# Optimization experiments

Hardware: AMD Instinct MI355X
Metric: run time of the kernel (lower is better)

## Reference

```python
import jax, jax.numpy as jnp
import numpy as np


def setup_inputs() -> dict:
    key = jax.random.key(0)
    ks = jax.random.split(key, 6)
    E, N, S = 6, 4096, 64
    std_b = (2.0 / (S + S)) ** 0.5
    std_a = (2.0 / (S + S)) ** 0.5
    return {
        "x": jax.random.normal(ks[0], (1, N, S), dtype=jnp.float32),
        "edge_matrix": jax.random.uniform(ks[1], (E, N, N), dtype=jnp.float32),
        "ba": jnp.zeros((S,), dtype=jnp.float32),
        "wz_wr_wh": jax.random.normal(ks[2], (E, S, 3 * S), dtype=jnp.float32) * std_b,
        "uz_ur": jax.random.normal(ks[3], (S, 2 * S), dtype=jnp.float32) * std_b,
        "uh": jax.random.normal(ks[4], (S, S), dtype=jnp.float32) * std_a,
        "iteration": 10,
    }


def reference(x, edge_matrix, ba, wz_wr_wh, uz_ur, uh, iteration):
    # x: [1, N, S]; edge_matrix: [E, N, N]; secondary_size == size branch.
    S = uh.shape[0]
    h = x[0]  # [N, S]

    def step(h, _):
        # activation[e] = edge_matrix[e]^T @ h + ba  -> [E, N, S]
        act = jnp.einsum('ejn,js->ens', edge_matrix, h) + ba
        # per-edge-type GRU projections, summed over edge types -> [N, 3S]
        zrh = jnp.einsum('ens,esk->nk', act, wz_wr_wh)
        wz, wr, wh = zrh[:, :S], zrh[:, S:2 * S], zrh[:, 2 * S:]
        uzr = h @ uz_ur  # [N, 2S]
        z = jax.nn.sigmoid(wz + uzr[:, :S])
        r = jax.nn.sigmoid(wr + uzr[:, S:])
        hh = jnp.tanh(wh + (r * h) @ uh)
        return (1.0 - z) * h + z * hh, None

    h, _ = jax.lax.scan(step, h, None, length=int(iteration))
    return h[None]  # [1, N, S]
```

## Files before the change

### kernel.cpp

```cpp
#include <hip/hip_runtime.h>
#include <cstdint>
#include <cstddef>

#define NN 4096
#define SS 64
#define EE 6
#define BN 64
#define KT 64
#define ITERS 10
#define NSG  128

typedef _Float16 f16x8 __attribute__((ext_vector_type(8)));
typedef float f32x4 __attribute__((ext_vector_type(4)));

__device__ __forceinline__ float sigf(float x) { return 1.0f / (1.0f + __expf(-x)); }

__device__ __forceinline__ size_t cb2(int e, int wt, int nh, int sg, int pl) {
    return (((((size_t)e * (NN / 32) + wt) * 2 + nh) * NSG + sg) * 2 + pl) * 512;
}
__device__ __forceinline__ size_t bidx(int sg, int st, int pl) {
    return (((size_t)sg * 4 + st) * 2 + pl) * 512;
}
__device__ __forceinline__ size_t bslot(int n, int s, int pl) {
    const int sg = n >> 5, jo = n & 31;
    const int lane = ((jo >> 3) << 4) | (s & 15);
    return bidx(sg, s >> 4, pl) + (size_t)lane * 8 + (jo & 7);
}

__global__ __launch_bounds__(256) void k_init(const float* __restrict__ x,
                                              float* __restrict__ h,
                                              _Float16* __restrict__ hTf,
                                              _Float16* __restrict__ hTh,
                                              _Float16* __restrict__ hTl) {
    const int t = threadIdx.x;
    const int n = blockIdx.x * 16 + (t & 15);
    const int c0 = (t >> 4) * 4;
    float4 v = *(const float4*)(x + (size_t)n * SS + c0);
    *(float4*)(h + (size_t)n * SS + c0) = v;
    const float vv[4] = {v.x, v.y, v.z, v.w};
#pragma unroll
    for (int k = 0; k < 4; k++) {
        _Float16 hi = (_Float16)vv[k];
        _Float16 lo = (_Float16)(vv[k] - (float)hi);
        if (hTf) {
            hTf[bslot(n, c0 + k, 0)] = hi;
            hTf[bslot(n, c0 + k, 1)] = lo;
        }
        if (hTh) {
            hTh[(size_t)(c0 + k) * NN + n] = hi;
            hTl[(size_t)(c0 + k) * NN + n] = lo;
        }
    }
}

__global__ __launch_bounds__(128, 4) void k_act_pack(const float* __restrict__ edge,
                                                     const _Float16* __restrict__ hTf,
                                                     float* __restrict__ act_part,
                                                     _Float16* __restrict__ eTf,
                                                     int jtot) {
    const int nt = blockIdx.x;
    const int e  = blockIdx.y;
    const int js = blockIdx.z;
    const int tid = threadIdx.x;
    const int w   = tid >> 6;
    const int lane = tid & 63;
    const int ln = lane & 15;
    const int lk = (lane >> 4) * 8;
    const int wt = nt * 2 + w;
    const int n0 = wt * 32;
    const int jbase = js * jtot;
    const int NSTEP = jtot / 32;
    const int sgbase = js * NSTEP;

    const float* A0 = edge + (size_t)e * NN * NN + (size_t)(jbase + lk) * NN + (n0 + ln);
    const float* A1 = A0 + 16;
    _Float16* stb0 = eTf + cb2(e, wt, 0, sgbase, 0) + (size_t)lane * 8;
    _Float16* stb1 = eTf + cb2(e, wt, 1, sgbase, 0) + (size_t)lane * 8;

    f32x4 acc[2][4];
#pragma unroll
    for (int nh = 0; nh < 2; nh++)
#pragma unroll
        for (int st = 0; st < 4; st++) acc[nh][st] = (f32x4)0.0f;

    f16x8 h0[2], l0[2], h1[2], l1[2];

#define LOADA(H, L, s_)                                                      \
    {                                                                        \
        const int sc = ((s_) < NSTEP) ? (s_) : 0;                            \
        const size_t off = (size_t)sc * 32 * NN;                             \
        float t0[8], t1[8];                                                  \
        _Pragma("unroll")                                                    \
        for (int i = 0; i < 8; i++) {                                        \
            t0[i] = A0[off + (size_t)i * NN];                                \
            t1[i] = A1[off + (size_t)i * NN];                                \
        }                                                                    \
        _Pragma("unroll")                                                    \
        for (int i = 0; i < 8; i++) {                                        \
            _Float16 hi0 = (_Float16)t0[i];                                  \
            H[0][i] = hi0;                                                   \
            L[0][i] = (_Float16)(t0[i] - (float)hi0);                        \
            _Float16 hi1 = (_Float16)t1[i];                                  \
            H[1][i] = hi1;                                                   \
            L[1][i] = (_Float16)(t1[i] - (float)hi1);                        \
        }                                                                    \
        _Float16* sp0 = stb0 + (size_t)sc * 1024;                            \
        *(f16x8*)(sp0)       = H[0];                                         \
        *(f16x8*)(sp0 + 512) = L[0];                                         \
        _Float16* sp1 = stb1 + (size_t)sc * 1024;                            \
        *(f16x8*)(sp1)       = H[1];                                         \
        *(f16x8*)(sp1 + 512) = L[1];                                         \
    }

#define COMPUTE(H, L, s)                                                     \
    {                                                                        \
        f16x8 bh[4], bl[4];                                                  \
        _Pragma("unroll")                                                    \
        for (int st = 0; st < 4; st++) {                                     \
            bh[st] = *(const f16x8*)(hTf + bidx(sgbase + (s), st, 0) + (size_t)lane * 8); \
            bl[st] = *(const f16x8*)(hTf + bidx(sgbase + (s), st, 1) + (size_t)lane * 8); \
        }                                                                    \
        _Pragma("unroll")                                                    \
        for (int nh = 0; nh < 2; nh++) {                                     \
            _Pragma("unroll")                                                \
            for (int st = 0; st < 4; st++) {                                 \
                acc[nh][st] = __builtin_amdgcn_mfma_f32_16x16x32_f16(        \
                    H[nh], bh[st], acc[nh][st], 0, 0, 0);                    \
                acc[nh][st] = __builtin_amdgcn_mfma_f32_16x16x32_f16(        \
                    H[nh], bl[st], acc[nh][st], 0, 0, 0);                    \
                acc[nh][st] = __builtin_amdgcn_mfma_f32_16x16x32_f16(        \
                    L[nh], bh[st], acc[nh][st], 0, 0, 0);                    \
            }                                                                \
        }                                                                    \
    }

    LOADA(h0, l0, 0);
    LOADA(h1, l1, 1);
    for (int s = 0; s < NSTEP; s += 2) {
        COMPUTE(h0, l0, s);     LOADA(h0, l0, s + 2);
        COMPUTE(h1, l1, s + 1); LOADA(h1, l1, s + 3);
    }
#undef LOADA
#undef COMPUTE

    float* ap = act_part + (size_t)(js * EE + e) * NN * SS;
#pragma unroll
    for (int nh = 0; nh < 2; nh++)
#pragma unroll
        for (int st = 0; st < 4; st++)
#pragma unroll
            for (int r = 0; r < 4; r++) {
                const int n = n0 + nh * 16 + (lane >> 4) * 4 + r;
                ap[(size_t)n * SS + st * 16 + ln] = acc[nh][st][r];
            }
}

__global__ __launch_bounds__(64, 6) void k_act4n(const _Float16* __restrict__ eTf,
                                                 const _Float16* __restrict__ hTf,
                                                 float* __restrict__ act_part,
                                                 int jtot) {
    const int bx = blockIdx.x;
    const int e  = blockIdx.y;
    const int js = blockIdx.z;
    const int wt = bx >> 1;
    const int nh = bx & 1;
    const int lane = threadIdx.x;
    const int ln = lane & 15;
    const int n0 = bx * 16;
    const int NSTEP = jtot / 32;
    const int sgbase = js * NSTEP;

    const _Float16* Abase = eTf + cb2(e, wt, nh, sgbase, 0) + (size_t)lane * 8;

    f32x4 acc[4];
#pragma unroll
    for (int st = 0; st < 4; st++) acc[st] = (f32x4)0.0f;

    f16x8 H0, L0, H1, L1;

#define LOADA(H, L, s_)                                                      \
    {                                                                        \
        const int sc = ((s_) < NSTEP) ? (s_) : 0;                            \
        const _Float16* p = Abase + (size_t)sc * 1024;                       \
        H = *(const f16x8*)(p);                                              \
        L = *(const f16x8*)(p + 512);                                        \
    }

#define COMPUTE(H, L, s)                                                     \
    {                                                                        \
        f16x8 bh[4], bl[4];                                                  \
        _Pragma("unroll")                                                    \
        for (int st = 0; st < 4; st++) {                                     \
            bh[st] = *(const f16x8*)(hTf + bidx(sgbase + (s), st, 0) + (size_t)lane * 8); \
            bl[st] = *(const f16x8*)(hTf + bidx(sgbase + (s), st, 1) + (size_t)lane * 8); \
        }                                                                    \
        _Pragma("unroll")                                                    \
        for (int st = 0; st < 4; st++) {                                     \
            acc[st] = __builtin_amdgcn_mfma_f32_16x16x32_f16(                \
                H, bh[st], acc[st], 0, 0, 0);                                \
            acc[st] = __builtin_amdgcn_mfma_f32_16x16x32_f16(                \
                H, bl[st], acc[st], 0, 0, 0);                                \
            acc[st] = __builtin_amdgcn_mfma_f32_16x16x32_f16(                \
                L, bh[st], acc[st], 0, 0, 0);                                \
        }                                                                    \
    }

    LOADA(H0, L0, 0);
    LOADA(H1, L1, 1);
    for (int s = 0; s < NSTEP; s += 2) {
        COMPUTE(H0, L0, s);     LOADA(H0, L0, s + 2);
        COMPUTE(H1, L1, s + 1); LOADA(H1, L1, s + 3);
    }
#undef LOADA
#undef COMPUTE

    float* ap = act_part + (size_t)(js * EE + e) * NN * SS;
#pragma unroll
    for (int st = 0; st < 4; st++)
#pragma unroll
        for (int r = 0; r < 4; r++) {
            const int n = n0 + (lane >> 4) * 4 + r;
            ap[(size_t)n * SS + st * 16 + ln] = acc[st][r];
        }
}

__global__ __launch_bounds__(128, 4) void k_act_mfma(const float* __restrict__ edge,
                                                     const _Float16* __restrict__ hTh,
                                                     const _Float16* __restrict__ hTl,
                                                     float* __restrict__ act_part,
                                                     int jtot) {
    const int nt = blockIdx.x;
    const int e  = blockIdx.y;
    const int js = blockIdx.z;
    const int tid = threadIdx.x;
    const int w   = tid >> 6;
    const int lane = tid & 63;
    const int ln = lane & 15;
    const int lk = (lane >> 4) * 8;
    const int n0 = nt * 64 + w * 32;
    const int jbase = js * jtot;
    const int NSTEP = jtot / 32;

    const float* A0 = edge + (size_t)e * NN * NN + (size_t)(jbase + lk) * NN + (n0 + ln);
    const float* A1 = A0 + 16;
    const size_t bbase = (size_t)ln * NN + jbase + lk;

    f32x4 acc[2][4];
#pragma unroll
    for (int nh = 0; nh < 2; nh++)
#pragma unroll
        for (int st = 0; st < 4; st++) acc[nh][st] = (f32x4)0.0f;

    f16x8 h0[2], l0[2], h1[2], l1[2];

#define LOADA(H, L, s_)                                                      \
    {                                                                        \
        const int sc = ((s_) < NSTEP) ? (s_) : 0;                            \
        const size_t off = (size_t)sc * 32 * NN;                             \
        float t0[8], t1[8];                                                  \
        _Pragma("unroll")                                                    \
        for (int i = 0; i < 8; i++) {                                        \
            t0[i] = A0[off + (size_t)i * NN];                                \
            t1[i] = A1[off + (size_t)i * NN];                                \
        }                                                                    \
        _Pragma("unroll")                                                    \
        for (int i = 0; i < 8; i++) {                                        \
            _Float16 hi0 = (_Float16)t0[i];                                  \
            H[0][i] = hi0;                                                   \
            L[0][i] = (_Float16)(t0[i] - (float)hi0);                        \
            _Float16 hi1 = (_Float16)t1[i];                                  \
            H[1][i] = hi1;                                                   \
            L[1][i] = (_Float16)(t1[i] - (float)hi1);                        \
        }                                                                    \
    }

#define COMPUTE(H, L, s)                                                     \
    {                                                                        \
        f16x8 bh[4], bl[4];                                                  \
        _Pragma("unroll")                                                    \
        for (int st = 0; st < 4; st++) {                                     \
            const size_t bo = bbase + (size_t)st * 16 * NN + (size_t)(s) * 32;\
            bh[st] = *(const f16x8*)(hTh + bo);                              \
            bl[st] = *(const f16x8*)(hTl + bo);                              \
        }                                                                    \
        _Pragma("unroll")                                                    \
        for (int nh = 0; nh < 2; nh++) {                                     \
            _Pragma("unroll")                                                \
            for (int st = 0; st < 4; st++) {                                 \
                acc[nh][st] = __builtin_amdgcn_mfma_f32_16x16x32_f16(        \
                    H[nh], bh[st], acc[nh][st], 0, 0, 0);                    \
                acc[nh][st] = __builtin_amdgcn_mfma_f32_16x16x32_f16(        \
                    H[nh], bl[st], acc[nh][st], 0, 0, 0);                    \
                acc[nh][st] = __builtin_amdgcn_mfma_f32_16x16x32_f16(        \
                    L[nh], bh[st], acc[nh][st], 0, 0, 0);                    \
            }                                                                \
        }                                                                    \
    }

    LOADA(h0, l0, 0);
    LOADA(h1, l1, 1);
    for (int s = 0; s < NSTEP; s += 2) {
        COMPUTE(h0, l0, s);     LOADA(h0, l0, s + 2);
        COMPUTE(h1, l1, s + 1); LOADA(h1, l1, s + 3);
    }
#undef LOADA
#undef COMPUTE

    float* ap = act_part + (size_t)(js * EE + e) * NN * SS;
#pragma unroll
    for (int nh = 0; nh < 2; nh++)
#pragma unroll
        for (int st = 0; st < 4; st++)
#pragma unroll
            for (int r = 0; r < 4; r++) {
                const int n = n0 + nh * 16 + (lane >> 4) * 4 + r;
                ap[(size_t)n * SS + st * 16 + ln] = acc[nh][st][r];
            }
}

__global__ __launch_bounds__(128) void k_act(const float* __restrict__ edge,
                                             const float* __restrict__ h,
                                             float* __restrict__ act_part,
                                             int jtot) {
    __shared__ float hbuf[2][KT][SS];
    const int nb = blockIdx.x;
    const int e  = blockIdx.y;
    const int js = blockIdx.z;
    const int tid = threadIdx.x;
    const int ng = tid & 7;
    const int sg = tid >> 3;
    const int n0 = nb * BN;
    const int s0 = sg * 4;
    const int jbase = js * jtot;

    const float4* hsrc4 = (const float4*)(h + (size_t)jbase * SS);

    float acc[8][4];
#pragma unroll
    for (int i = 0; i < 8; i++)
#pragma unroll
        for (int k = 0; k < 4; k++) acc[i][k] = 0.0f;

    float4 pre[8];
#pragma unroll
    for (int r = 0; r < 8; r++) pre[r] = hsrc4[r * 128 + tid];
    {
        float4* dst = (float4*)&hbuf[0][0][0];
#pragma unroll
        for (int r = 0; r < 8; r++) dst[r * 128 + tid] = pre[r];
    }
    __syncthreads();

    const float* eg = edge + (size_t)e * NN * NN + (size_t)jbase * NN + n0 + ng * 8;

    float4 ea[4][2];
#pragma unroll
    for (int u = 0; u < 4; u++) {
        ea[u][0] = *(const float4*)(eg + (size_t)u * NN);
        ea[u][1] = *(const float4*)(eg + (size_t)u * NN + 4);
    }

    const int NCH = jtot / KT;
    for (int c = 0; c < NCH; c++) {
        if (c + 1 < NCH) {
#pragma unroll
            for (int r = 0; r < 8; r++) pre[r] = hsrc4[(c + 1) * (KT * SS / 4) + r * 128 + tid];
        }
        const float (*hb)[SS] = hbuf[c & 1];
        for (int jj = 0; jj < KT; jj += 4) {
            const int q = c * KT + jj + 4;
            const float* pe = eg + (size_t)(q < jtot ? q : 0) * NN;
            float4 eb[4][2];
#pragma unroll
            for (int u = 0; u < 4; u++) {
                eb[u][0] = *(const float4*)(pe + (size_t)u * NN);
                eb[u][1] = *(const float4*)(pe + (size_t)u * NN + 4);
            }
#pragma unroll
            for (int u = 0; u < 4; u++) {
                const float4 hv = *(const float4*)&hb[jj + u][s0];
                const float ev[8] = {ea[u][0].x, ea[u][0].y, ea[u][0].z, ea[u][0].w,
                                     ea[u][1].x, ea[u][1].y, ea[u][1].z, ea[u][1].w};
#pragma unroll
                for (int i = 0; i < 8; i++) {
                    acc[i][0] += ev[i] * hv.x;
                    acc[i][1] += ev[i] * hv.y;
                    acc[i][2] += ev[i] * hv.z;
                    acc[i][3] += ev[i] * hv.w;
                }
            }
#pragma unroll
            for (int u = 0; u < 4; u++) { ea[u][0] = eb[u][0]; ea[u][1] = eb[u][1]; }
        }
        if (c + 1 < NCH) {
            float4* dst = (float4*)&hbuf[(c + 1) & 1][0][0];
#pragma unroll
            for (int r = 0; r < 8; r++) dst[r * 128 + tid] = pre[r];
        }
        __syncthreads();
    }

    float* ap = act_part + (((size_t)js * EE + e) * NN + n0 + ng * 8) * SS + s0;
#pragma unroll
    for (int i = 0; i < 8; i++)
        *(float4*)(ap + (size_t)i * SS) = make_float4(acc[i][0], acc[i][1], acc[i][2], acc[i][3]);
}

__global__ __launch_bounds__(256) void k_update(const float* __restrict__ act_part,
                                                float* __restrict__ h,
                                                const float* __restrict__ W,
                                                const float* __restrict__ uz_ur,
                                                const float* __restrict__ uh,
                                                const float* __restrict__ ba,
                                                _Float16* __restrict__ hTf,
                                                _Float16* __restrict__ hTh,
                                                _Float16* __restrict__ hTl,
                                                int jparts) {
    __shared__ float w_lds[SS][192];
    __shared__ float a_lds[16][68];
    __shared__ float h_lds[16][68];
    __shared__ float zrh_lds[16][196];
    __shared__ float uzr_lds[16][132];
    __shared__ float rh_lds[16][68];

    const int n0 = blockIdx.x * 16;
    const int t = threadIdx.x;
    const int nl = t & 15;
    const int kg = t >> 4;

    {
        const int row = t >> 4, c4 = t & 15;
        float4 v = *(const float4*)(h + (size_t)(n0 + row) * SS + c4 * 4);
        *(float4*)&h_lds[row][c4 * 4] = v;
    }

    float zacc[12];
#pragma unroll
    for (int k = 0; k < 12; k++) zacc[k] = 0.0f;
    const int k0 = kg * 12;

    for (int e = 0; e < EE; e++) {
        __syncthreads();
        {
            const float4* wsrc = (const float4*)(W + (size_t)e * SS * 192);
            float4* wdst = (float4*)&w_lds[0][0];
#pragma unroll
            for (int r = 0; r < 12; r++) wdst[r * 256 + t] = wsrc[r * 256 + t];
        }
        {
            const int row = t >> 4, c4 = t & 15;
            const size_t base = ((size_t)e * NN + (n0 + row)) * SS + c4 * 4;
            float4 bv = *(const float4*)(ba + c4 * 4);
            float vx = bv.x, vy = bv.y, vz = bv.z, vw = bv.w;
            for (int p = 0; p < jparts; p++) {
                float4 pp = *(const float4*)(act_part + base + (size_t)p * EE * NN * SS);
                vx += pp.x; vy += pp.y; vz += pp.z; vw += pp.w;
            }
            *(float4*)&a_lds[row][c4 * 4] = make_float4(vx, vy, vz, vw);
        }
        __syncthreads();
#pragma unroll 8
        for (int s = 0; s < SS; s++) {
            const float av = a_lds[nl][s];
            const float4* wrow = (const float4*)&w_lds[s][k0];
            const float4 w0 = wrow[0], w1 = wrow[1], w2 = wrow[2];
            zacc[0] += av * w0.x; zacc[1] += av * w0.y; zacc[2]  += av * w0.z; zacc[3]  += av * w0.w;
            zacc[4] += av * w1.x; zacc[5] += av * w1.y; zacc[6]  += av * w1.z; zacc[7]  += av * w1.w;
            zacc[8] += av * w2.x; zacc[9] += av * w2.y; zacc[10] += av * w2.z; zacc[11] += av * w2.w;
        }
    }

    float uacc[8];
#pragma unroll
    for (int k = 0; k < 8; k++) uacc[k] = 0.0f;
#pragma unroll 4
    for (int j = 0; j < SS; j++) {
        const float hv = h_lds[nl][j];
        const float4* urow = (const float4*)(uz_ur + (size_t)j * 128 + kg * 8);
        const float4 u0 = urow[0], u1 = urow[1];
        uacc[0] += hv * u0.x; uacc[1] += hv * u0.y; uacc[2] += hv * u0.z; uacc[3] += hv * u0.w;
        uacc[4] += hv * u1.x; uacc[5] += hv * u1.y; uacc[6] += hv * u1.z; uacc[7] += hv * u1.w;
    }

    *(float4*)&zrh_lds[nl][k0]     = make_float4(zacc[0], zacc[1], zacc[2], zacc[3]);
    *(float4*)&zrh_lds[nl][k0 + 4] = make_float4(zacc[4], zacc[5], zacc[6], zacc[7]);
    *(float4*)&zrh_lds[nl][k0 + 8] = make_float4(zacc[8], zacc[9], zacc[10], zacc[11]);
    *(float4*)&uzr_lds[nl][kg * 8]     = make_float4(uacc[0], uacc[1], uacc[2], uacc[3]);
    *(float4*)&uzr_lds[nl][kg * 8 + 4] = make_float4(uacc[4], uacc[5], uacc[6], uacc[7]);
    __syncthreads();

    const int sg4 = kg * 4;
    const float4 wz = *(const float4*)&zrh_lds[nl][sg4];
    const float4 wr = *(const float4*)&zrh_lds[nl][64 + sg4];
    const float4 wh = *(const float4*)&zrh_lds[nl][128 + sg4];
    const float4 uz = *(const float4*)&uzr_lds[nl][sg4];
    const float4 ur = *(const float4*)&uzr_lds[nl][64 + sg4];
    const float4 hv4 = *(const float4*)&h_lds[nl][sg4];

    float z4[4], rh4[4];
    {
        const float wzv[4] = {wz.x, wz.y, wz.z, wz.w};
        const float wrv[4] = {wr.x, wr.y, wr.z, wr.w};
        const float uzv[4] = {uz.x, uz.y, uz.z, uz.w};
        const float urv[4] = {ur.x, ur.y, ur.z, ur.w};
        const float hvv[4] = {hv4.x, hv4.y, hv4.z, hv4.w};
#pragma unroll
        for (int k = 0; k < 4; k++) {
            z4[k] = sigf(wzv[k] + uzv[k]);
            const float r = sigf(wrv[k] + urv[k]);
            rh4[k] = r * hvv[k];
        }
    }
    *(float4*)&rh_lds[nl][sg4] = make_float4(rh4[0], rh4[1], rh4[2], rh4[3]);
    __syncthreads();

    float hacc[4];
#pragma unroll
    for (int k = 0; k < 4; k++) hacc[k] = 0.0f;
#pragma unroll 4
    for (int j = 0; j < SS; j++) {
        const float rhv = rh_lds[nl][j];
        const float4 u = *(const float4*)(uh + (size_t)j * SS + sg4);
        hacc[0] += rhv * u.x; hacc[1] += rhv * u.y; hacc[2] += rhv * u.z; hacc[3] += rhv * u.w;
    }

    {
        const float whv[4] = {wh.x, wh.y, wh.z, wh.w};
        const float hvv[4] = {hv4.x, hv4.y, hv4.z, hv4.w};
        float ov[4];
#pragma unroll
        for (int k = 0; k < 4; k++) {
            const float hh = tanhf(whv[k] + hacc[k]);
            ov[k] = (1.0f - z4[k]) * hvv[k] + z4[k] * hh;
        }
        const int n = n0 + nl;
        *(float4*)(h + (size_t)n * SS + sg4) = make_float4(ov[0], ov[1], ov[2], ov[3]);
#pragma unroll
        for (int k = 0; k < 4; k++) {
            _Float16 hi = (_Float16)ov[k];
            _Float16 lo = (_Float16)(ov[k] - (float)hi);
            if (hTf) {
                hTf[bslot(n, sg4 + k, 0)] = hi;
                hTf[bslot(n, sg4 + k, 1)] = lo;
            }
            if (hTh) {
                hTh[(size_t)(sg4 + k) * NN + n] = hi;
                hTl[(size_t)(sg4 + k) * NN + n] = lo;
            }
        }
    }
}

extern "C" void kernel_launch(void* const* d_in, const int* in_sizes, int n_in,
                              void* d_out, int out_size, void* d_ws, size_t ws_size,
                              hipStream_t stream) {
    const float* x    = (const float*)d_in[0];
    const float* edge = (const float*)d_in[1];
    const float* ba   = (const float*)d_in[2];
    const float* W    = (const float*)d_in[3];
    const float* uzur = (const float*)d_in[4];
    const float* uh   = (const float*)d_in[5];

    float* h = (float*)d_out;
    char*  wsb = (char*)d_ws;

    const size_t actB = (size_t)EE * NN * SS * sizeof(float);
    const size_t hTfB = (size_t)NSG * 4 * 2 * 512 * sizeof(_Float16);
    const size_t hTBu = (size_t)SS * NN * sizeof(_Float16) * 2;
    const size_t eTfB = (size_t)EE * NN * NN * 2 * sizeof(_Float16);
    const int jp = 4;
    const size_t needFull = eTfB + (size_t)jp * actB + hTfB;

    if (ws_size >= needFull) {
        _Float16* eTf = (_Float16*)wsb;
        float*    act = (float*)(wsb + eTfB);
        _Float16* hTf = (_Float16*)(wsb + eTfB + (size_t)jp * actB);
        const int jtot = NN / jp;

        k_init<<<NN / 16, 256, 0, stream>>>(x, h, hTf, nullptr, nullptr);

        k_act_pack<<<dim3(NN / 64, EE, jp), 128, 0, stream>>>(edge, hTf, act, eTf, jtot);
        k_update<<<NN / 16, 256, 0, stream>>>(act, h, W, uzur, uh, ba, hTf, nullptr, nullptr, jp);

        for (int it = 1; it < ITERS; ++it) {
            k_act4n<<<dim3(NN / 16, EE, jp), 64, 0, stream>>>(eTf, hTf, act, jtot);
            k_update<<<NN / 16, 256, 0, stream>>>(act, h, W, uzur, uh, ba, hTf, nullptr, nullptr, jp);
        }
    } else {
        int jp2;
        bool use_mfma;
        if      (ws_size >= 4 * actB + hTBu) { jp2 = 4; use_mfma = true;  }
        else if (ws_size >= 2 * actB + hTBu) { jp2 = 2; use_mfma = true;  }
        else if (ws_size >= 1 * actB + hTBu) { jp2 = 1; use_mfma = true;  }
        else                                 { jp2 = 1; use_mfma = false; }

        float*     act = (float*)wsb;
        _Float16*  hTh = use_mfma ? (_Float16*)(wsb + (size_t)jp2 * actB) : nullptr;
        _Float16*  hTl = use_mfma ? (_Float16*)(wsb + (size_t)jp2 * actB) + (size_t)SS * NN : nullptr;
        const int jtot = NN / jp2;

        k_init<<<NN / 16, 256, 0, stream>>>(x, h, nullptr, hTh, hTl);
        for (int it = 0; it < ITERS; ++it) {
            if (use_mfma) {
                k_act_mfma<<<dim3(NN / 64, EE, jp2), 128, 0, stream>>>(edge, hTh, hTl, act, jtot);
            } else {
                k_act<<<dim3(NN / BN, EE, jp2), 128, 0, stream>>>(edge, h, act, jtot);
            }
            k_update<<<NN / 16, 256, 0, stream>>>(act, h, W, uzur, uh, ba, nullptr, hTh, hTl, jp2);
        }
    }
}
```

Before: 1.739 ms.

## Widen per-wave N tile to 64 rows and relayout packed edge matrix

Repacks the cached fp16 hi/lo edge matrix into 64-row chunks per k-step and replaces the 16-row-per-wave act kernel with one where each wave computes 64 rows. Each hT B-fragment load is then reused across four MFMA row tiles instead of one, cutting redundant loads of hT. The trade-off is four times fewer waves in the grid and a much larger accumulator/register footprint, with launch bounds lowered accordingly, which reduces occupancy and latency hiding.

```diff
diff --git a/kernel.cpp b/kernel.cpp
--- a/kernel.cpp
+++ b/kernel.cpp
@@ -15,8 +15,8 @@
 
 __device__ __forceinline__ float sigf(float x) { return 1.0f / (1.0f + __expf(-x)); }
 
-__device__ __forceinline__ size_t cb2(int e, int wt, int nh, int sg, int pl) {
-    return (((((size_t)e * (NN / 32) + wt) * 2 + nh) * NSG + sg) * 2 + pl) * 512;
+__device__ __forceinline__ size_t cb64(int e, int wt, int sg, int q) {
+    return ((((size_t)e * (NN / 64) + wt) * NSG + sg) * 8 + q) * 512;
 }
 __device__ __forceinline__ size_t bidx(int sg, int st, int pl) {
     return (((size_t)sg * 4 + st) * 2 + pl) * 512;
@@ -66,16 +66,15 @@
     const int lane = tid & 63;
     const int ln = lane & 15;
     const int lk = (lane >> 4) * 8;
-    const int wt = nt * 2 + w;
-    const int n0 = wt * 32;
+    const int n0 = nt * 64 + w * 32;
     const int jbase = js * jtot;
     const int NSTEP = jtot / 32;
     const int sgbase = js * NSTEP;
 
     const float* A0 = edge + (size_t)e * NN * NN + (size_t)(jbase + lk) * NN + (n0 + ln);
     const float* A1 = A0 + 16;
-    _Float16* stb0 = eTf + cb2(e, wt, 0, sgbase, 0) + (size_t)lane * 8;
-    _Float16* stb1 = eTf + cb2(e, wt, 1, sgbase, 0) + (size_t)lane * 8;
+    _Float16* stb0 = eTf + cb64(e, nt, sgbase, (w * 2 + 0) * 2) + (size_t)lane * 8;
+    _Float16* stb1 = eTf + cb64(e, nt, sgbase, (w * 2 + 1) * 2) + (size_t)lane * 8;
 
     f32x4 acc[2][4];
 #pragma unroll
@@ -104,10 +103,10 @@
             H[1][i] = hi1;                                                   \
             L[1][i] = (_Float16)(t1[i] - (float)hi1);                        \
         }                                                                    \
-        _Float16* sp0 = stb0 + (size_t)sc * 1024;                            \
+        _Float16* sp0 = stb0 + (size_t)sc * 4096;                            \
         *(f16x8*)(sp0)       = H[0];                                         \
         *(f16x8*)(sp0 + 512) = L[0];                                         \
-        _Float16* sp1 = stb1 + (size_t)sc * 1024;                            \
+        _Float16* sp1 = stb1 + (size_t)sc * 4096;                            \
         *(f16x8*)(sp1)       = H[1];                                         \
         *(f16x8*)(sp1 + 512) = L[1];                                         \
     }
@@ -155,35 +154,38 @@
             }
 }
 
-__global__ __launch_bounds__(64, 6) void k_act4n(const _Float16* __restrict__ eTf,
+__global__ __launch_bounds__(64, 2) void k_act4w(const _Float16* __restrict__ eTf,
                                                  const _Float16* __restrict__ hTf,
                                                  float* __restrict__ act_part,
                                                  int jtot) {
-    const int bx = blockIdx.x;
+    const int wt = blockIdx.x;
     const int e  = blockIdx.y;
     const int js = blockIdx.z;
-    const int wt = bx >> 1;
-    const int nh = bx & 1;
     const int lane = threadIdx.x;
     const int ln = lane & 15;
-    const int n0 = bx * 16;
+    const int n0 = wt * 64;
     const int NSTEP = jtot / 32;
     const int sgbase = js * NSTEP;
 
-    const _Float16* Abase = eTf + cb2(e, wt, nh, sgbase, 0) + (size_t)lane * 8;
-
-    f32x4 acc[4];
-#pragma unroll
-    for (int st = 0; st < 4; st++) acc[st] = (f32x4)0.0f;
-
-    f16x8 H0, L0, H1, L1;
+    const _Float16* Abase = eTf + cb64(e, wt, sgbase, 0) + (size_t)lane * 8;
+
+    f32x4 acc[4][4];
+#pragma unroll
+    for (int qt = 0; qt < 4; qt++)
+#pragma unroll
+        for (int st = 0; st < 4; st++) acc[qt][st] = (f32x4)0.0f;
+
+    f16x8 H0[4], L0[4], H1[4], L1[4];
 
 #define LOADA(H, L, s_)                                                      \
     {                                                                        \
         const int sc = ((s_) < NSTEP) ? (s_) : 0;                            \
-        const _Float16* p = Abase + (size_t)sc * 1024;                       \
-        H = *(const f16x8*)(p);                                              \
-        L = *(const f16x8*)(p + 512);                                        \
+        const _Float16* p = Abase + (size_t)sc * 4096;                       \
+        _Pragma("unroll")                                                    \
+        for (int qt = 0; qt < 4; qt++) {                                     \
+            H[qt] = *(const f16x8*)(p + qt * 1024);                          \
+            L[qt] = *(const f16x8*)(p + qt * 1024 + 512);                    \
+        }                                                                    \
     }
 
 #define COMPUTE(H, L, s)                                                     \
@@ -195,13 +197,16 @@
             bl[st] = *(const f16x8*)(hTf + bidx(sgbase + (s), st, 1) + (size_t)lane * 8); \
         }                                                                    \
         _Pragma("unroll")                                                    \
-        for (int st = 0; st < 4; st++) {                                     \
-            acc[st] = __builtin_amdgcn_mfma_f32_16x16x32_f16(                \
-                H, bh[st], acc[st], 0, 0, 0);                                \
-            acc[st] = __builtin_amdgcn_mfma_f32_16x16x32_f16(                \
-                H, bl[st], acc[st], 0, 0, 0);                                \
-            acc[st] = __builtin_amdgcn_mfma_f32_16x16x32_f16(                \
-                L, bh[st], acc[st], 0, 0, 0);                                \
+        for (int qt = 0; qt < 4; qt++) {                                     \
+            _Pragma("unroll")                                                \
+            for (int st = 0; st < 4; st++) {                                 \
+                acc[qt][st] = __builtin_amdgcn_mfma_f32_16x16x32_f16(        \
+                    H[qt], bh[st], acc[qt][st], 0, 0, 0);                    \
+                acc[qt][st] = __builtin_amdgcn_mfma_f32_16x16x32_f16(        \
+                    H[qt], bl[st], acc[qt][st], 0, 0, 0);                    \
+                acc[qt][st] = __builtin_amdgcn_mfma_f32_16x16x32_f16(        \
+                    L[qt], bh[st], acc[qt][st], 0, 0, 0);                    \
+            }                                                                \
         }                                                                    \
     }
 
@@ -216,12 +221,14 @@
 
     float* ap = act_part + (size_t)(js * EE + e) * NN * SS;
 #pragma unroll
-    for (int st = 0; st < 4; st++)
-#pragma unroll
-        for (int r = 0; r < 4; r++) {
-            const int n = n0 + (lane >> 4) * 4 + r;
-            ap[(size_t)n * SS + st * 16 + ln] = acc[st][r];
-        }
+    for (int qt = 0; qt < 4; qt++)
+#pragma unroll
+        for (int st = 0; st < 4; st++)
+#pragma unroll
+            for (int r = 0; r < 4; r++) {
+                const int n = n0 + qt * 16 + (lane >> 4) * 4 + r;
+                ap[(size_t)n * SS + st * 16 + ln] = acc[qt][st][r];
+            }
 }
 
 __global__ __launch_bounds__(128, 4) void k_act_mfma(const float* __restrict__ edge,
@@ -583,7 +590,7 @@
         k_update<<<NN / 16, 256, 0, stream>>>(act, h, W, uzur, uh, ba, hTf, nullptr, nullptr, jp);
 
         for (int it = 1; it < ITERS; ++it) {
-            k_act4n<<<dim3(NN / 16, EE, jp), 64, 0, stream>>>(eTf, hTf, act, jtot);
+            k_act4w<<<dim3(NN / 64, EE, jp), 64, 0, stream>>>(eTf, hTf, act, jtot);
             k_update<<<NN / 16, 256, 0, stream>>>(act, h, W, uzur, uh, ba, hTf, nullptr, nullptr, jp);
         }
     } else {
```

Measured after the change: 1.422 ms (median of 2 runs). 1.22x faster.
